# Performance work log

Hardware: AMD Instinct MI355X
Metric: run time of the kernel (lower is better)

## Reference

```python
import jax, jax.numpy as jnp
import numpy as np

B, H, S, D = 2, 8, 2048, 64
ALPHA = 1
P_NORM = 2
EPS = 1e-5


def setup_inputs() -> dict:
    key = jax.random.key(0)
    kq, kk, kv = jax.random.split(key, 3)
    query = jax.random.normal(kq, (B, H, S, D), dtype=jnp.float32)
    keys = jax.random.normal(kk, (B, H, S, D), dtype=jnp.float32)
    vals = jax.random.normal(kv, (B, H, S, D), dtype=jnp.float32)
    # causal mask: 1 where attention allowed, 0 elsewhere (masked_fill on mask==0)
    mask = jnp.tril(jnp.ones((S, S), dtype=jnp.int32))[None, None, :, :]
    return {"query": query, "keys": keys, "vals": vals, "mask": mask}


def reference(query, keys, vals, mask):
    d = query.shape[-1]
    sqrt_d = jnp.asarray(d, query.dtype) ** 0.5
    # L2-normalized cosine similarity term
    q_n = query / jnp.linalg.norm(query, axis=-1, keepdims=True)
    k_n = keys / jnp.linalg.norm(keys, axis=-1, keepdims=True)
    cos = jnp.einsum('bhqd,bhkd->bhqk', q_n, k_n)
    rq = (1.0 + (1.0 - cos) / (ALPHA * sqrt_d)) ** (-ALPHA)
    preattn = jnp.log(rq + EPS)
    # magnitude term: (||q||_p^p + ||k||_p^p) / (2 sqrt(d))
    q_mag = jnp.sum(jnp.abs(query) ** P_NORM, axis=-1, keepdims=True)  # [B,H,S,1]
    k_mag = jnp.sum(jnp.abs(keys) ** P_NORM, axis=-1, keepdims=True)   # [B,H,S,1]
    preattn = preattn + (q_mag + jnp.swapaxes(k_mag, -2, -1)) / (2.0 * sqrt_d)
    preattn = jnp.where(mask == 0, -jnp.inf, preattn)
    attn = jax.nn.softmax(preattn, axis=-1)
    out = jnp.einsum('bhqk,bhkd->bhqd', attn, vals)
    return out, attn
```

## Files before the change

### kernel.cpp

```cpp
#include <hip/hip_runtime.h>
#include <math.h>


#define BH 16
#define SS 2048
#define DD 64
#define NKT 32

typedef float f4a __attribute__((ext_vector_type(4)));
typedef short bs8 __attribute__((ext_vector_type(8)));
typedef short bs4 __attribute__((ext_vector_type(4)));
typedef unsigned int u32x2 __attribute__((ext_vector_type(2)));

__device__ __forceinline__ short bf16rne(float f) {
  unsigned u = __float_as_uint(f);
  u += 0x7fffu + ((u >> 16) & 1u);
  return (short)(u >> 16);
}
__device__ __forceinline__ float truncb(float x) {
  return __uint_as_float(__float_as_uint(x) & 0xffff0000u);
}
__device__ __forceinline__ unsigned packhi(float lo, float hi) {
  return (__float_as_uint(hi) & 0xffff0000u) | (__float_as_uint(lo) >> 16);
}

__device__ __forceinline__ f4a mfma16(bs4 a, bs4 b, f4a c) {
#if __has_builtin(__builtin_amdgcn_mfma_f32_16x16x16bf16_1k)
  return __builtin_amdgcn_mfma_f32_16x16x16bf16_1k(a, b, c, 0, 0, 0);
#else
  f4a d;
  asm("v_mfma_f32_16x16x16_bf16 %0, %1, %2, %3"
      : "=v"(d)
      : "v"(a), "v"(b), "v"(c));
  return d;
#endif
}

__device__ __forceinline__ int kunit(int kc, int dgrp) {
  return ((kc >> 2) & 3) | (((dgrp >> 1) & 1) << 2) | ((dgrp & 1) << 3) |
         ((kc & 3) << 4) | ((kc >> 4) << 6);
}

__global__ __launch_bounds__(256) void rq_rowss(const float* __restrict__ q,
                                                const float* __restrict__ k,
                                                float* __restrict__ ws) {
  int gid = blockIdx.x * 256 + threadIdx.x;
  int grp = gid >> 4;
  int lane = gid & 15;
  const int nrows = BH * SS;
  const float* src = (grp < nrows) ? q : k;
  int row = (grp < nrows) ? grp : (grp - nrows);
  float4 v = *(const float4*)(src + (size_t)row * DD + lane * 4);
  float s = v.x * v.x + v.y * v.y + v.z * v.z + v.w * v.w;
  s += __shfl_xor(s, 1);
  s += __shfl_xor(s, 2);
  s += __shfl_xor(s, 4);
  s += __shfl_xor(s, 8);
  if (lane == 0) ws[grp] = s;
}

__global__ __launch_bounds__(512, 4) void rq_attn(const float* __restrict__ Q,
                                                  const float* __restrict__ K,
                                                  const float* __restrict__ V,
                                                  const float* __restrict__ ss,
                                                  float* __restrict__ outp,
                                                  float* __restrict__ attnp) {
  __shared__ short smemS[12288];
  __shared__ float aBuf[64 * 68];
  __shared__ float ektS[64];
  __shared__ float lrowp[2][64];
  __shared__ float lrow[64];
  short* const Kf = smemS;
  short* const VtH = smemS + 4096;
  short* const VtL = smemS + 8192;

  const int t = threadIdx.x;
  const int bx = blockIdx.x;
  const int qt = NKT - 1 - (bx >> 4);
  const int bh = bx & 15;
  const int qbase = qt * 64;
  const float* Qg = Q + (size_t)bh * SS * DD;
  const float* Kg = K + (size_t)bh * SS * DD;
  const float* Vg = V + (size_t)bh * SS * DD;
  float* Ag = attnp + (size_t)bh * SS * SS;
  const float* qss = ss + (size_t)bh * SS;
  const float* kss = ss + (size_t)(BH * SS) + (size_t)bh * SS;

  const int l = t & 63;
  const int wid = t >> 6;
  const int qq = wid >> 1;
  const int kch = wid & 1;
  const int l15 = l & 15;
  const int lh = l >> 4;

  const int ukb = kunit(l15, lh) * 8;

  const int p1_kc = t >> 3;
  const int p1_df = t & 7;
  const int p1_ks = p1_df >> 2;
  const int p1_addr = p1_ks * 2048 + kunit(p1_kc, p1_df & 3) * 8;

  auto stageK_unit = [&](int kbase, int kc, int df, int addr) {
    const float* src = Kg + (size_t)(kbase + kc) * DD + df * 8;
    float4 x = *(const float4*)src;
    float4 y = *(const float4*)(src + 4);
    float rn = rsqrtf(kss[kbase + kc]);
    bs8 b;
    b[0] = bf16rne(x.x * rn);
    b[1] = bf16rne(x.y * rn);
    b[2] = bf16rne(x.z * rn);
    b[3] = bf16rne(x.w * rn);
    b[4] = bf16rne(y.x * rn);
    b[5] = bf16rne(y.y * rn);
    b[6] = bf16rne(y.z * rn);
    b[7] = bf16rne(y.w * rn);
    *(bs8*)&Kf[addr] = b;
  };

  const int g_row = t >> 3;
  const int g_c0 = (t & 7) << 2;
  auto gatherStoreA = [&](int kt) {
#pragma unroll
    for (int it = 0; it < 2; ++it) {
      const int col = g_c0 + it * 32;
      f4a v = *(const f4a*)&aBuf[g_row * 68 + col];
      __builtin_nontemporal_store(
          v, (f4a*)(Ag + (size_t)(qbase + g_row) * SS + kt * 64 + col));
    }
  };

  const int s_rb = ((t & 255) >> 4) << 2;
  const int s_c0 = (t & 15) << 2;
  const int kgw = (t & 255) >> 4;

  bs8 qf[2];
  {
    const int row = qbase + qq * 16 + l15;
    const float rn = rsqrtf(qss[row]);
#pragma unroll
    for (int ks = 0; ks < 2; ++ks) {
      const float* src = Qg + (size_t)row * DD + ks * 32 + lh * 8;
      float4 x = *(const float4*)src;
      float4 y = *(const float4*)(src + 4);
      bs8 q;
      q[0] = bf16rne(x.x * rn);
      q[1] = bf16rne(x.y * rn);
      q[2] = bf16rne(x.z * rn);
      q[3] = bf16rne(x.w * rn);
      q[4] = bf16rne(y.x * rn);
      q[5] = bf16rne(y.y * rn);
      q[6] = bf16rne(y.z * rn);
      q[7] = bf16rne(y.w * rn);
      qf[ks] = q;
    }
  }

  const f4a fz = {0.f, 0.f, 0.f, 0.f};

  float rs = 0.f;
  for (int kt = 0; kt <= qt; ++kt) {
    const int kbase = kt * 64;
    stageK_unit(kbase, p1_kc, p1_df, p1_addr);
    if (t < 64) ektS[t] = __expf(kss[kbase + t] * 0.0625f);
    __syncthreads();

    f4a acc[2];
    acc[0] = fz;
    acc[1] = fz;
#pragma unroll
    for (int ks = 0; ks < 2; ++ks)
#pragma unroll
      for (int nb = 0; nb < 2; ++nb) {
        bs8 kf = *(const bs8*)&Kf[ks * 2048 + ((kch * 2 + nb) << 9) + ukb];
        acc[nb] = __builtin_amdgcn_mfma_f32_16x16x32_bf16(kf, qf[ks], acc[nb],
                                                          0, 0, 0);
      }

    const bool diag = (kt == qt);
    const int qg = qq * 16 + l15;
#pragma unroll
    for (int nb = 0; nb < 2; ++nb)
#pragma unroll
      for (int r = 0; r < 4; ++r) {
        const int kg = kch * 32 + nb * 16 + lh * 4 + r;
        float w = fmaf(8.0f, __builtin_amdgcn_rcpf(9.0f - acc[nb][r]), 1e-5f) *
                  ektS[kg];
        if (diag && kg > qg) w = 0.0f;
        rs += w;
      }
    __syncthreads();
  }

  rs += __shfl_xor(rs, 16);
  rs += __shfl_xor(rs, 32);
  if (l < 16) lrowp[kch][qq * 16 + l15] = rs;
  __syncthreads();
  if (t < 64) lrow[t] = 1.0f / (lrowp[0][t] + lrowp[1][t]);
  __syncthreads();
  const float li = lrow[qq * 16 + l15];

  f4a O[4];
#pragma unroll
  for (int i = 0; i < 4; ++i) O[i] = fz;

  for (int kt = 0; kt <= qt; ++kt) {
    const int kbase = kt * 64;
    if (kt > 0) gatherStoreA(kt - 1);
    if (t < 256) {
      float mm[4][4];
#pragma unroll
      for (int i = 0; i < 4; ++i)
        *(float4*)&mm[i][0] =
            *(const float4*)(Vg + (size_t)(kbase + s_rb + i) * DD + s_c0);
#pragma unroll
      for (int j = 0; j < 4; ++j) {
        const int d = s_c0 + j;
        const int si = (d * 16 + (kgw ^ (d & 15))) * 4;
        u32x2 h, lo2;
        h.x = packhi(mm[0][j], mm[1][j]);
        h.y = packhi(mm[2][j], mm[3][j]);
        float r0 = mm[0][j] - truncb(mm[0][j]);
        float r1 = mm[1][j] - truncb(mm[1][j]);
        float r2 = mm[2][j] - truncb(mm[2][j]);
        float r3 = mm[3][j] - truncb(mm[3][j]);
        lo2.x = packhi(r0, r1);
        lo2.y = packhi(r2, r3);
        *(u32x2*)&VtH[si] = h;
        *(u32x2*)&VtL[si] = lo2;
      }
      if (t < 64) ektS[t] = __expf(kss[kbase + t] * 0.0625f);
    } else {
      const int tp = t - 256;
      const int kc = tp >> 2;
      const int df0 = (tp & 3) << 1;
#pragma unroll
      for (int u = 0; u < 2; ++u) {
        const int df = df0 + u;
        stageK_unit(kbase, kc, df, (df >> 2) * 2048 + kunit(kc, df & 3) * 8);
      }
    }
    __syncthreads();

    f4a acc[2];
    acc[0] = fz;
    acc[1] = fz;
#pragma unroll
    for (int ks = 0; ks < 2; ++ks)
#pragma unroll
      for (int nb = 0; nb < 2; ++nb) {
        bs8 kf = *(const bs8*)&Kf[ks * 2048 + ((kch * 2 + nb) << 9) + ukb];
        acc[nb] = __builtin_amdgcn_mfma_f32_16x16x32_bf16(kf, qf[ks], acc[nb],
                                                          0, 0, 0);
      }

    u32x2 pH[2], pL[2];
    const bool diag = (kt == qt);
    const int qg = qq * 16 + l15;
#pragma unroll
    for (int nb = 0; nb < 2; ++nb) {
      float av[4];
#pragma unroll
      for (int r = 0; r < 4; ++r) {
        const int kg = kch * 32 + nb * 16 + lh * 4 + r;
        float w = fmaf(8.0f, __builtin_amdgcn_rcpf(9.0f - acc[nb][r]), 1e-5f) *
                  ektS[kg];
        if (diag && kg > qg) w = 0.0f;
        av[r] = w * li;
      }
      f4a a4 = {av[0], av[1], av[2], av[3]};
      *(f4a*)&aBuf[qg * 68 + kch * 32 + nb * 16 + lh * 4] = a4;
      pH[nb].x = packhi(av[0], av[1]);
      pH[nb].y = packhi(av[2], av[3]);
      float r0 = av[0] - truncb(av[0]);
      float r1 = av[1] - truncb(av[1]);
      float r2 = av[2] - truncb(av[2]);
      float r3 = av[3] - truncb(av[3]);
      pL[nb].x = packhi(r0, r1);
      pL[nb].y = packhi(r2, r3);
    }

#pragma unroll
    for (int nb = 0; nb < 2; ++nb) {
      const int kg = kch * 8 + nb * 4 + lh;
      bs4 VH[4], VL[4];
#pragma unroll
      for (int db = 0; db < 4; ++db) {
        const int d = db * 16 + l15;
        const int si = (d * 16 + (kg ^ (d & 15))) * 4;
        VH[db] = *(const bs4*)&VtH[si];
        VL[db] = *(const bs4*)&VtL[si];
      }
      const bs4 AH = __builtin_bit_cast(bs4, pH[nb]);
      const bs4 AL = __builtin_bit_cast(bs4, pL[nb]);
#pragma unroll
      for (int db = 0; db < 4; ++db) O[db] = mfma16(AH, VH[db], O[db]);
#pragma unroll
      for (int db = 0; db < 4; ++db) O[db] = mfma16(AH, VL[db], O[db]);
#pragma unroll
      for (int db = 0; db < 4; ++db) O[db] = mfma16(AL, VH[db], O[db]);
    }
    __syncthreads();
  }

  gatherStoreA(qt);

  {
    const f4a z = {0.f, 0.f, 0.f, 0.f};
    const int r0i = (t >> 4) << 1;
    const int c0i = (t & 15) << 2;
    for (int kt = qt + 1; kt < NKT; ++kt) {
#pragma unroll
      for (int i = 0; i < 2; ++i)
        __builtin_nontemporal_store(
            z, (f4a*)(Ag + (size_t)(qbase + r0i + i) * SS + kt * 64 + c0i));
    }
  }

  float* Osc = (float*)smemS;
  if (kch == 1) {
#pragma unroll
    for (int db = 0; db < 4; ++db)
#pragma unroll
      for (int r = 0; r < 4; ++r)
        Osc[(qq * 16 + lh * 4 + r) * 64 + db * 16 + l15] = O[db][r];
  }
  __syncthreads();
  if (kch == 0) {
    float* Og = outp + (size_t)bh * SS * DD;
#pragma unroll
    for (int db = 0; db < 4; ++db)
#pragma unroll
      for (int r = 0; r < 4; ++r) {
        const int row = qq * 16 + lh * 4 + r;
        Og[(size_t)(qbase + row) * DD + db * 16 + l15] =
            O[db][r] + Osc[row * 64 + db * 16 + l15];
      }
  }
}

extern "C" void kernel_launch(void* const* d_in, const int* in_sizes, int n_in,
                              void* d_out, int out_size, void* d_ws, size_t ws_size,
                              hipStream_t stream) {
  const float* q = (const float*)d_in[0];
  const float* k = (const float*)d_in[1];
  const float* v = (const float*)d_in[2];
  float* out = (float*)d_out;
  float* attn = out + (size_t)BH * SS * DD;
  float* ws = (float*)d_ws;

  rq_rowss<<<dim3((2 * BH * SS) / 16), dim3(256), 0, stream>>>(q, k, ws);
  rq_attn<<<dim3(NKT * 16), dim3(512), 0, stream>>>(q, k, v, ws, out, attn);
}
```

Before: 400.7 us.

## Halve query tile to 32 rows and register-prefetch next K/V tile

Measured after the change: 375.3 us. -6.3%, faster.

```diff
diff --git a/kernel.cpp b/kernel.cpp
--- a/kernel.cpp
+++ b/kernel.cpp
@@ -5,7 +5,6 @@
 #define BH 16
 #define SS 2048
 #define DD 64
-#define NKT 32
 
 typedef float f4a __attribute__((ext_vector_type(4)));
 typedef short bs8 __attribute__((ext_vector_type(8)));
@@ -59,26 +58,35 @@
   if (lane == 0) ws[grp] = s;
 }
 
-__global__ __launch_bounds__(512, 4) void rq_attn(const float* __restrict__ Q,
+struct KS {
+  float4 a, b, c, d;
+  float ss;
+};
+struct VS {
+  float4 m0, m1, m2, m3;
+};
+
+__global__ __launch_bounds__(256, 4) void rq_attn(const float* __restrict__ Q,
                                                   const float* __restrict__ K,
                                                   const float* __restrict__ V,
                                                   const float* __restrict__ ss,
                                                   float* __restrict__ outp,
                                                   float* __restrict__ attnp) {
   __shared__ short smemS[12288];
-  __shared__ float aBuf[64 * 68];
+  __shared__ float aBuf[32 * 68];
   __shared__ float ektS[64];
-  __shared__ float lrowp[2][64];
-  __shared__ float lrow[64];
+  __shared__ float lrowp[2][32];
+  __shared__ float lrow[32];
   short* const Kf = smemS;
   short* const VtH = smemS + 4096;
   short* const VtL = smemS + 8192;
 
   const int t = threadIdx.x;
   const int bx = blockIdx.x;
-  const int qt = NKT - 1 - (bx >> 4);
+  const int qt32 = 63 - (bx >> 4);
   const int bh = bx & 15;
-  const int qbase = qt * 64;
+  const int qbase = qt32 * 32;
+  const int nkt = (qt32 >> 1) + 1;
   const float* Qg = Q + (size_t)bh * SS * DD;
   const float* Kg = K + (size_t)bh * SS * DD;
   const float* Vg = V + (size_t)bh * SS * DD;
@@ -95,26 +103,78 @@
 
   const int ukb = kunit(l15, lh) * 8;
 
-  const int p1_kc = t >> 3;
-  const int p1_df = t & 7;
-  const int p1_ks = p1_df >> 2;
-  const int p1_addr = p1_ks * 2048 + kunit(p1_kc, p1_df & 3) * 8;
-
-  auto stageK_unit = [&](int kbase, int kc, int df, int addr) {
-    const float* src = Kg + (size_t)(kbase + kc) * DD + df * 8;
-    float4 x = *(const float4*)src;
-    float4 y = *(const float4*)(src + 4);
-    float rn = rsqrtf(kss[kbase + kc]);
-    bs8 b;
-    b[0] = bf16rne(x.x * rn);
-    b[1] = bf16rne(x.y * rn);
-    b[2] = bf16rne(x.z * rn);
-    b[3] = bf16rne(x.w * rn);
-    b[4] = bf16rne(y.x * rn);
-    b[5] = bf16rne(y.y * rn);
-    b[6] = bf16rne(y.z * rn);
-    b[7] = bf16rne(y.w * rn);
-    *(bs8*)&Kf[addr] = b;
+  const int kc_s = t >> 2;
+  const int df0_s = (t & 3) << 1;
+  const int kaddr0 = (df0_s >> 2) * 2048 + kunit(kc_s, df0_s & 3) * 8;
+  const int kaddr1 = ((df0_s + 1) >> 2) * 2048 + kunit(kc_s, (df0_s + 1) & 3) * 8;
+
+  auto loadK = [&](int kbase) {
+    KS r;
+    const float* src = Kg + (size_t)(kbase + kc_s) * DD + df0_s * 8;
+    r.a = *(const float4*)(src + 0);
+    r.b = *(const float4*)(src + 4);
+    r.c = *(const float4*)(src + 8);
+    r.d = *(const float4*)(src + 12);
+    r.ss = kss[kbase + kc_s];
+    return r;
+  };
+  auto writeK = [&](const KS& r) {
+    const float rn = rsqrtf(r.ss);
+    bs8 u0, u1;
+    u0[0] = bf16rne(r.a.x * rn);
+    u0[1] = bf16rne(r.a.y * rn);
+    u0[2] = bf16rne(r.a.z * rn);
+    u0[3] = bf16rne(r.a.w * rn);
+    u0[4] = bf16rne(r.b.x * rn);
+    u0[5] = bf16rne(r.b.y * rn);
+    u0[6] = bf16rne(r.b.z * rn);
+    u0[7] = bf16rne(r.b.w * rn);
+    u1[0] = bf16rne(r.c.x * rn);
+    u1[1] = bf16rne(r.c.y * rn);
+    u1[2] = bf16rne(r.c.z * rn);
+    u1[3] = bf16rne(r.c.w * rn);
+    u1[4] = bf16rne(r.d.x * rn);
+    u1[5] = bf16rne(r.d.y * rn);
+    u1[6] = bf16rne(r.d.z * rn);
+    u1[7] = bf16rne(r.d.w * rn);
+    *(bs8*)&Kf[kaddr0] = u0;
+    *(bs8*)&Kf[kaddr1] = u1;
+  };
+
+  const int s_rb = (t >> 4) << 2;
+  const int s_c0 = (t & 15) << 2;
+  const int kgw = t >> 4;
+
+  auto loadV = [&](int kbase) {
+    VS r;
+    r.m0 = *(const float4*)(Vg + (size_t)(kbase + s_rb + 0) * DD + s_c0);
+    r.m1 = *(const float4*)(Vg + (size_t)(kbase + s_rb + 1) * DD + s_c0);
+    r.m2 = *(const float4*)(Vg + (size_t)(kbase + s_rb + 2) * DD + s_c0);
+    r.m3 = *(const float4*)(Vg + (size_t)(kbase + s_rb + 3) * DD + s_c0);
+    return r;
+  };
+  auto writeV = [&](const VS& r) {
+    float mm[4][4];
+    *(float4*)&mm[0][0] = (float4){r.m0.x, r.m0.y, r.m0.z, r.m0.w};
+    *(float4*)&mm[1][0] = (float4){r.m1.x, r.m1.y, r.m1.z, r.m1.w};
+    *(float4*)&mm[2][0] = (float4){r.m2.x, r.m2.y, r.m2.z, r.m2.w};
+    *(float4*)&mm[3][0] = (float4){r.m3.x, r.m3.y, r.m3.z, r.m3.w};
+#pragma unroll
+    for (int j = 0; j < 4; ++j) {
+      const int d = s_c0 + j;
+      const int si = (d * 16 + (kgw ^ (d & 15))) * 4;
+      u32x2 h, lo2;
+      h.x = packhi(mm[0][j], mm[1][j]);
+      h.y = packhi(mm[2][j], mm[3][j]);
+      float r0 = mm[0][j] - truncb(mm[0][j]);
+      float r1 = mm[1][j] - truncb(mm[1][j]);
+      float r2 = mm[2][j] - truncb(mm[2][j]);
+      float r3 = mm[3][j] - truncb(mm[3][j]);
+      lo2.x = packhi(r0, r1);
+      lo2.y = packhi(r2, r3);
+      *(u32x2*)&VtH[si] = h;
+      *(u32x2*)&VtL[si] = lo2;
+    }
   };
 
   const int g_row = t >> 3;
@@ -129,17 +189,13 @@
     }
   };
 
-  const int s_rb = ((t & 255) >> 4) << 2;
-  const int s_c0 = (t & 15) << 2;
-  const int kgw = (t & 255) >> 4;
-
+  const int qglob = qbase + qq * 16 + l15;
   bs8 qf[2];
   {
-    const int row = qbase + qq * 16 + l15;
-    const float rn = rsqrtf(qss[row]);
+    const float rn = rsqrtf(qss[qglob]);
 #pragma unroll
     for (int ks = 0; ks < 2; ++ks) {
-      const float* src = Qg + (size_t)row * DD + ks * 32 + lh * 8;
+      const float* src = Qg + (size_t)qglob * DD + ks * 32 + lh * 8;
       float4 x = *(const float4*)src;
       float4 y = *(const float4*)(src + 4);
       bs8 q;
@@ -157,12 +213,18 @@
 
   const f4a fz = {0.f, 0.f, 0.f, 0.f};
 
+  KS kreg = loadK(0);
+  float ekraw = (t < 64) ? kss[t] : 0.f;
   float rs = 0.f;
-  for (int kt = 0; kt <= qt; ++kt) {
+  for (int kt = 0; kt < nkt; ++kt) {
     const int kbase = kt * 64;
-    stageK_unit(kbase, p1_kc, p1_df, p1_addr);
-    if (t < 64) ektS[t] = __expf(kss[kbase + t] * 0.0625f);
+    writeK(kreg);
+    if (t < 64) ektS[t] = __expf(ekraw * 0.0625f);
     __syncthreads();
+    if (kt + 1 < nkt) {
+      kreg = loadK(kbase + 64);
+      if (t < 64) ekraw = kss[kbase + 64 + t];
+    }
 
     f4a acc[2];
     acc[0] = fz;
@@ -176,8 +238,7 @@
                                                           0, 0, 0);
       }
 
-    const bool diag = (kt == qt);
-    const int qg = qq * 16 + l15;
+    const bool diag = (kt == nkt - 1);
 #pragma unroll
     for (int nb = 0; nb < 2; ++nb)
 #pragma unroll
@@ -185,7 +246,7 @@
         const int kg = kch * 32 + nb * 16 + lh * 4 + r;
         float w = fmaf(8.0f, __builtin_amdgcn_rcpf(9.0f - acc[nb][r]), 1e-5f) *
                   ektS[kg];
-        if (diag && kg > qg) w = 0.0f;
+        if (diag && (kbase + kg) > qglob) w = 0.0f;
         rs += w;
       }
     __syncthreads();
@@ -195,7 +256,7 @@
   rs += __shfl_xor(rs, 32);
   if (l < 16) lrowp[kch][qq * 16 + l15] = rs;
   __syncthreads();
-  if (t < 64) lrow[t] = 1.0f / (lrowp[0][t] + lrowp[1][t]);
+  if (t < 32) lrow[t] = 1.0f / (lrowp[0][t] + lrowp[1][t]);
   __syncthreads();
   const float li = lrow[qq * 16 + l15];
 
@@ -203,43 +264,22 @@
 #pragma unroll
   for (int i = 0; i < 4; ++i) O[i] = fz;
 
-  for (int kt = 0; kt <= qt; ++kt) {
+  kreg = loadK(0);
+  VS vreg = loadV(0);
+  if (t < 64) ekraw = kss[t];
+
+  for (int kt = 0; kt < nkt; ++kt) {
     const int kbase = kt * 64;
     if (kt > 0) gatherStoreA(kt - 1);
-    if (t < 256) {
-      float mm[4][4];
-#pragma unroll
-      for (int i = 0; i < 4; ++i)
-        *(float4*)&mm[i][0] =
-            *(const float4*)(Vg + (size_t)(kbase + s_rb + i) * DD + s_c0);
-#pragma unroll
-      for (int j = 0; j < 4; ++j) {
-        const int d = s_c0 + j;
-        const int si = (d * 16 + (kgw ^ (d & 15))) * 4;
-        u32x2 h, lo2;
-        h.x = packhi(mm[0][j], mm[1][j]);
-        h.y = packhi(mm[2][j], mm[3][j]);
-        float r0 = mm[0][j] - truncb(mm[0][j]);
-        float r1 = mm[1][j] - truncb(mm[1][j]);
-        float r2 = mm[2][j] - truncb(mm[2][j]);
-        float r3 = mm[3][j] - truncb(mm[3][j]);
-        lo2.x = packhi(r0, r1);
-        lo2.y = packhi(r2, r3);
-        *(u32x2*)&VtH[si] = h;
-        *(u32x2*)&VtL[si] = lo2;
-      }
-      if (t < 64) ektS[t] = __expf(kss[kbase + t] * 0.0625f);
-    } else {
-      const int tp = t - 256;
-      const int kc = tp >> 2;
-      const int df0 = (tp & 3) << 1;
-#pragma unroll
-      for (int u = 0; u < 2; ++u) {
-        const int df = df0 + u;
-        stageK_unit(kbase, kc, df, (df >> 2) * 2048 + kunit(kc, df & 3) * 8);
-      }
-    }
+    writeV(vreg);
+    writeK(kreg);
+    if (t < 64) ektS[t] = __expf(ekraw * 0.0625f);
     __syncthreads();
+    if (kt + 1 < nkt) {
+      kreg = loadK(kbase + 64);
+      vreg = loadV(kbase + 64);
+      if (t < 64) ekraw = kss[kbase + 64 + t];
+    }
 
     f4a acc[2];
     acc[0] = fz;
@@ -254,7 +294,7 @@
       }
 
     u32x2 pH[2], pL[2];
-    const bool diag = (kt == qt);
+    const bool diag = (kt == nkt - 1);
     const int qg = qq * 16 + l15;
 #pragma unroll
     for (int nb = 0; nb < 2; ++nb) {
@@ -264,7 +304,7 @@
         const int kg = kch * 32 + nb * 16 + lh * 4 + r;
         float w = fmaf(8.0f, __builtin_amdgcn_rcpf(9.0f - acc[nb][r]), 1e-5f) *
                   ektS[kg];
-        if (diag && kg > qg) w = 0.0f;
+        if (diag && (kbase + kg) > qglob) w = 0.0f;
         av[r] = w * li;
       }
       f4a a4 = {av[0], av[1], av[2], av[3]};
@@ -302,17 +342,16 @@
     __syncthreads();
   }
 
-  gatherStoreA(qt);
+  gatherStoreA(nkt - 1);
 
   {
     const f4a z = {0.f, 0.f, 0.f, 0.f};
-    const int r0i = (t >> 4) << 1;
-    const int c0i = (t & 15) << 2;
-    for (int kt = qt + 1; kt < NKT; ++kt) {
-#pragma unroll
-      for (int i = 0; i < 2; ++i)
+    for (int kt = nkt; kt < 32; ++kt) {
+#pragma unroll
+      for (int it = 0; it < 2; ++it)
         __builtin_nontemporal_store(
-            z, (f4a*)(Ag + (size_t)(qbase + r0i + i) * SS + kt * 64 + c0i));
+            z, (f4a*)(Ag + (size_t)(qbase + g_row) * SS + kt * 64 + g_c0 +
+                      it * 32));
     }
   }
 
@@ -349,5 +388,5 @@
   float* ws = (float*)d_ws;
 
   rq_rowss<<<dim3((2 * BH * SS) / 16), dim3(256), 0, stream>>>(q, k, ws);
-  rq_attn<<<dim3(NKT * 16), dim3(512), 0, stream>>>(q, k, v, ws, out, attn);
-}
+  rq_attn<<<dim3(64 * 16), dim3(256), 0, stream>>>(q, k, v, ws, out, attn);
+}
```
